# Kernel optimization log

Hardware: AMD Instinct MI355X
Metric: run time of the kernel (lower is better)

The kernel has to match this reference:

```python
import jax, jax.numpy as jnp
import numpy as np

B_, T_, DIN, H, DZ, DX = 64, 256, 128, 256, 8, 8


def setup_inputs() -> dict:
    key = jax.random.key(0)
    ks = jax.random.split(key, 13)
    p = lambda k, sh: jax.random.normal(k, sh, dtype=jnp.float32) * 0.05
    return {
        "y": jax.random.normal(ks[0], (B_, T_, DIN), dtype=jnp.float32),
        "W_ih": p(ks[1], (3 * H, DIN)), "W_hh": p(ks[2], (3 * H, H)),
        "b_ih": p(ks[3], (3 * H,)), "b_hh": p(ks[4], (3 * H,)),
        "W_mz": p(ks[5], (DZ, H)), "b_mz": p(ks[6], (DZ,)),
        "W_mx": p(ks[7], (DX, H)), "b_mx": p(ks[8], (DX,)),
        "W_pz": p(ks[9], (2 * DZ, H)), "b_pz": p(ks[10], (2 * DZ,)),
        "W_cx": p(ks[11], (DX * DX, H)), "b_cx": p(ks[12], (DX * DX,)),
    }


def _gru(y, W_ih, W_hh, b_ih, b_hh):
    # torch nn.GRU (single layer, unidirectional, batch_first)
    B, T, _ = y.shape
    Hh = W_hh.shape[1]
    x_proj = jnp.einsum('btd,gd->btg', y, W_ih) + b_ih  # [B,T,3H]

    def step(h, xp):
        hp = h @ W_hh.T + b_hh
        xr, xz, xn = jnp.split(xp, 3, axis=-1)
        hr, hz, hn = jnp.split(hp, 3, axis=-1)
        r = jax.nn.sigmoid(xr + hr)
        z = jax.nn.sigmoid(xz + hz)
        n = jnp.tanh(xn + r * hn)
        h_new = (1.0 - z) * n + z * h
        return h_new, h_new

    h0 = jnp.zeros((B, Hh), dtype=y.dtype)
    _, hs = jax.lax.scan(step, h0, jnp.swapaxes(x_proj, 0, 1))
    return jnp.swapaxes(hs, 0, 1)  # [B,T,H]


def _forward(y, W_ih, W_hh, b_ih, b_hh, W_mz, b_mz, W_mx, b_mx, W_pz, b_pz, W_cx, b_cx):
    enc = _gru(y, W_ih, W_hh, b_ih, b_hh)                       # [B,T,H]
    mean_z = enc @ W_mz.T + b_mz                                 # [B,T,DZ]
    mean_x = enc @ W_mx.T + b_mx                                 # [B,T,DX]
    bd_z = enc @ W_pz.T + b_pz                                   # [B,T,2*DZ]  (apply_softplus=False)

    # banded cov: per latent dim, upper-bidiagonal cholesky factor [B,T,T]
    diag = jnp.moveaxis(jax.nn.softplus(bd_z[..., :DZ]), -1, 0)  # [DZ,B,T]
    off = jnp.moveaxis(bd_z[:, :-1, DZ:], -1, 0)                 # [DZ,B,T-1]
    B, T = diag.shape[1], diag.shape[2]
    idx = jnp.arange(T)
    chol_z = (jnp.zeros((DZ, B, T, T), dtype=y.dtype)
              .at[:, :, idx, idx].set(diag)
              .at[:, :, idx[:-1], idx[1:]].set(off))             # [DZ,B,T,T]

    # anchor first two x-dims at t=0 (in-place mutation in torch)
    mean_x = mean_x.at[:, :, :2].add(-mean_x[:, 0:1, :2])
    mean_x_flat = mean_x.reshape(B * T, DX)

    cov_x = enc @ W_cx.T + b_cx                                  # [B,T,DX*DX]
    cov_x_flat = cov_x.reshape(B * T, DX, DX)
    return mean_z, chol_z, mean_x_flat, cov_x_flat


def reference(y, W_ih, W_hh, b_ih, b_hh, W_mz, b_mz, W_mx, b_mx, W_pz, b_pz, W_cx, b_cx):
    return _forward(y, W_ih, W_hh, b_ih, b_hh, W_mz, b_mz, W_mx, b_mx, W_pz, b_pz, W_cx, b_cx)
```

## Files before the change

kernel.cpp:

```cpp
#include <hip/hip_runtime.h>
#include <cstdint>
#include <cstddef>

#define B_   64
#define T_   256
#define DIN_ 128
#define H_   256
#define G3_  768

typedef _Float16 f16x8 __attribute__((ext_vector_type(8)));
typedef float    f32x4 __attribute__((ext_vector_type(4)));

#define MFMA(a, b, c) __builtin_amdgcn_mfma_f32_16x16x32_f16((a), (b), (c), 0, 0, 0)

__device__ __forceinline__ unsigned short f2h(float f) {
  _Float16 h = (_Float16)f;
  return __builtin_bit_cast(unsigned short, h);
}

__global__ __launch_bounds__(256) void prep_kernel(
    const float* __restrict__ W_ih, const float* __restrict__ W_hh,
    const float* __restrict__ W_mz, const float* __restrict__ W_mx,
    const float* __restrict__ W_pz, const float* __restrict__ W_cx,
    float* __restrict__ WT_ih, float* __restrict__ WheadT,
    unsigned* __restrict__ Wreg) {
  int i = blockIdx.x * 256 + threadIdx.x;
  if (i < 98304) {
    int k = i / 768, g = i % 768;
    WT_ih[i] = W_ih[g * 128 + k];
  } else if (i < 98304 + 24576) {
    int j = i - 98304;
    int c = j >> 8, k = j & 255;
    float v;
    if (c < 8)       v = W_mz[c * 256 + k];
    else if (c < 16) v = W_mx[(c - 8) * 256 + k];
    else if (c < 32) v = W_pz[(c - 16) * 256 + k];
    else             v = W_cx[(c - 32) * 256 + k];
    WheadT[j] = v;
  } else {
    int m = i - 122880;
    int c = m & 3, n = m >> 2;
    int tid = n & 511, j4 = n >> 9;
    int g   = j4 >> 4;
    int rem = j4 & 15;
    int uti = rem >> 3, kf = rem & 7;
    int wv = tid >> 6, l = tid & 63;
    int u = (2 * wv + uti) * 16 + (l & 15);
    int k = kf * 32 + ((l >> 4) << 3) + 2 * c;
    int row = g * 256 + u;
    unsigned short lo = f2h(W_hh[row * 256 + k]);
    unsigned short hi = f2h(W_hh[row * 256 + k + 1]);
    Wreg[m] = ((unsigned)hi << 16) | (unsigned)lo;
  }
}

__global__ __launch_bounds__(256) void xproj_kernel(
    const float* __restrict__ y, const float* __restrict__ WT_ih,
    const float* __restrict__ b_ih, const float* __restrict__ b_hh,
    float* __restrict__ xp) {
  __shared__ float ylds[64][132];
  int tid = threadIdx.x;
  int row0 = blockIdx.x * 64;
  const float4* y4 = (const float4*)(y + (size_t)row0 * DIN_);
#pragma unroll
  for (int i = 0; i < 8; ++i) {
    int idx = i * 256 + tid;
    float4 v = y4[idx];
    int r = idx >> 5, c4 = (idx & 31) * 4;
    ylds[r][c4 + 0] = v.x; ylds[r][c4 + 1] = v.y;
    ylds[r][c4 + 2] = v.z; ylds[r][c4 + 3] = v.w;
  }
  __syncthreads();
  int tx = tid & 15, ty = tid >> 4;
  for (int c = 0; c < 6; ++c) {
    int col0 = c * 128 + tx * 8;
    float acc[4][8];
#pragma unroll
    for (int a = 0; a < 4; ++a)
#pragma unroll
      for (int b = 0; b < 8; ++b) acc[a][b] = 0.f;
#pragma unroll 4
    for (int k = 0; k < 128; ++k) {
      float4 w0 = *(const float4*)&WT_ih[k * 768 + col0];
      float4 w1 = *(const float4*)&WT_ih[k * 768 + col0 + 4];
      float a0 = ylds[ty * 4 + 0][k], a1 = ylds[ty * 4 + 1][k];
      float a2 = ylds[ty * 4 + 2][k], a3 = ylds[ty * 4 + 3][k];
      acc[0][0] += a0 * w0.x; acc[0][1] += a0 * w0.y; acc[0][2] += a0 * w0.z; acc[0][3] += a0 * w0.w;
      acc[0][4] += a0 * w1.x; acc[0][5] += a0 * w1.y; acc[0][6] += a0 * w1.z; acc[0][7] += a0 * w1.w;
      acc[1][0] += a1 * w0.x; acc[1][1] += a1 * w0.y; acc[1][2] += a1 * w0.z; acc[1][3] += a1 * w0.w;
      acc[1][4] += a1 * w1.x; acc[1][5] += a1 * w1.y; acc[1][6] += a1 * w1.z; acc[1][7] += a1 * w1.w;
      acc[2][0] += a2 * w0.x; acc[2][1] += a2 * w0.y; acc[2][2] += a2 * w0.z; acc[2][3] += a2 * w0.w;
      acc[2][4] += a2 * w1.x; acc[2][5] += a2 * w1.y; acc[2][6] += a2 * w1.z; acc[2][7] += a2 * w1.w;
      acc[3][0] += a3 * w0.x; acc[3][1] += a3 * w0.y; acc[3][2] += a3 * w0.z; acc[3][3] += a3 * w0.w;
      acc[3][4] += a3 * w1.x; acc[3][5] += a3 * w1.y; acc[3][6] += a3 * w1.z; acc[3][7] += a3 * w1.w;
    }
    float4 b0 = *(const float4*)&b_ih[col0];
    float4 b1 = *(const float4*)&b_ih[col0 + 4];
    if (c < 4) {
      float4 h0 = *(const float4*)&b_hh[col0];
      float4 h1 = *(const float4*)&b_hh[col0 + 4];
      b0.x += h0.x; b0.y += h0.y; b0.z += h0.z; b0.w += h0.w;
      b1.x += h1.x; b1.y += h1.y; b1.z += h1.z; b1.w += h1.w;
    }
#pragma unroll
    for (int a = 0; a < 4; ++a) {
      int row = row0 + ty * 4 + a;
      float4 o0, o1;
      o0.x = acc[a][0] + b0.x; o0.y = acc[a][1] + b0.y; o0.z = acc[a][2] + b0.z; o0.w = acc[a][3] + b0.w;
      o1.x = acc[a][4] + b1.x; o1.y = acc[a][5] + b1.y; o1.z = acc[a][6] + b1.z; o1.w = acc[a][7] + b1.w;
      *(float4*)&xp[(size_t)row * G3_ + col0] = o0;
      *(float4*)&xp[(size_t)row * G3_ + col0 + 4] = o1;
    }
  }
}

#define GRU_STEP(PAR, xr0, xz0, xn0, xr1, xz1, xn1,                            \
                 nxr0, nxz0, nxn0, nxr1, nxz1, nxn1)                           \
  {                                                                            \
    asm volatile("" ::: "memory");            \
    const int tc = t + PAR;                                                    \
    const float* xq = xpb + (size_t)(tc + 1) * G3_;          \
    nxr0 = xq[u0]; nxz0 = xq[256 + u0]; nxn0 = xq[512 + u0];                   \
    nxr1 = xq[u1]; nxz1 = xq[256 + u1]; nxn1 = xq[512 + u1];                   \
    uint4 hq0 = h4[PAR * 32 + g16];                                            \
    f16x8 hf0 = __builtin_bit_cast(f16x8, hq0);                                \
    f32x4 aR0 = MFMA(hf0, wf[0],  z4);  f32x4 aR1 = MFMA(hf0, wf[8],  z4);     \
    f32x4 aZ0 = MFMA(hf0, wf[16], z4);  f32x4 aZ1 = MFMA(hf0, wf[24], z4);     \
    f32x4 aN0 = MFMA(hf0, wf[32], z4);  f32x4 aN1 = MFMA(hf0, wf[40], z4);     \
    _Pragma("unroll")                                                          \
    for (int kf = 1; kf < 8; ++kf) {                                           \
      uint4 hq = h4[PAR * 32 + kf * 4 + g16];                                  \
      f16x8 hk = __builtin_bit_cast(f16x8, hq);                                \
      aR0 = MFMA(hk, wf[kf],      aR0); aR1 = MFMA(hk, wf[8 + kf],  aR1);      \
      aZ0 = MFMA(hk, wf[16 + kf], aZ0); aZ1 = MFMA(hk, wf[24 + kf], aZ1);      \
      aN0 = MFMA(hk, wf[32 + kf], aN0); aN1 = MFMA(hk, wf[40 + kf], aN1);      \
    }                                                                          \
    float pr0 = aR0[0] + xr0, pz0 = aZ0[0] + xz0, pn0 = aN0[0] + bhn0;         \
    float pr1 = aR1[0] + xr1, pz1 = aZ1[0] + xz1, pn1 = aN1[0] + bhn1;         \
    float r0 = 1.f / (1.f + __expf(-pr0)), r1 = 1.f / (1.f + __expf(-pr1));    \
    float q0 = 1.f / (1.f + __expf(-pz0)), q1 = 1.f / (1.f + __expf(-pz1));    \
    float a0 = xn0 + r0 * pn0, a1 = xn1 + r1 * pn1;                            \
    a0 = fminf(15.f, fmaxf(-15.f, a0)); a1 = fminf(15.f, fmaxf(-15.f, a1));    \
    float e0 = __expf(2.f * a0), e1 = __expf(2.f * a1);                        \
    float n0 = (e0 - 1.f) / (e0 + 1.f), n1 = (e1 - 1.f) / (e1 + 1.f);          \
    float h0n = (1.f - q0) * n0 + q0 * hold0;                                  \
    float h1n = (1.f - q1) * n1 + q1 * hold1;                                  \
    hold0 = h0n; hold1 = h1n;                 \
    if ((l >> 4) == 0) {                        \
      encb[tc * 256 + u0] = h0n;  encb[tc * 256 + u1] = h1n;                   \
      h16[PAR ^ 1][u0] = f2h(h0n); h16[PAR ^ 1][u1] = f2h(h1n);                \
    }                                                                          \
    __syncthreads();                                                           \
  }

__global__ __launch_bounds__(512) __attribute__((amdgpu_waves_per_eu(2, 2)))
void gru_kernel(
    const float* __restrict__ xp, const unsigned* Wreg,
    const float* __restrict__ b_hh, float* enc) {
  int tid = threadIdx.x;
  int b = blockIdx.x;
  int w = tid >> 6;
  int l = tid & 63;
  int g16 = l >> 4;
  int u0 = w * 32 + (l & 15);
  int u1 = u0 + 16;
  __shared__ alignas(16) unsigned short h16[2][256];

  f16x8 wf[48];
  const uint4* W4 = (const uint4*)Wreg;
#pragma unroll
  for (int fi = 0; fi < 48; ++fi) {
    uint4 q = W4[fi * 512 + tid];
    wf[fi] = __builtin_bit_cast(f16x8, q);
  }
  if (tid < 32) {
    uint4 z = {0u, 0u, 0u, 0u};
    ((uint4*)h16)[tid] = z;
  }
  const float* xpb = xp + (size_t)b * (T_ * G3_);
  float* encb = enc + (size_t)b * (T_ * H_);
  float bhn0 = b_hh[512 + u0], bhn1 = b_hh[512 + u1];
  float hold0 = 0.f, hold1 = 0.f;
  const f32x4 z4 = {0.f, 0.f, 0.f, 0.f};
  float xrA0 = xpb[u0], xzA0 = xpb[256 + u0], xnA0 = xpb[512 + u0];
  float xrA1 = xpb[u1], xzA1 = xpb[256 + u1], xnA1 = xpb[512 + u1];
  __syncthreads();
  const uint4* h4 = (const uint4*)h16;
  float xrB0, xzB0, xnB0, xrB1, xzB1, xnB1;
  for (int t = 0; t < T_; t += 2) {
    GRU_STEP(0, xrA0, xzA0, xnA0, xrA1, xzA1, xnA1,
                xrB0, xzB0, xnB0, xrB1, xzB1, xnB1)
    GRU_STEP(1, xrB0, xzB0, xnB0, xrB1, xzB1, xnB1,
                xrA0, xzA0, xnA0, xrA1, xzA1, xnA1)
  }
}

__global__ __launch_bounds__(384) void heads_kernel(
    const float* __restrict__ enc, const float* __restrict__ WheadT,
    const float* __restrict__ b_mz, const float* __restrict__ b_mx,
    const float* __restrict__ b_pz, const float* __restrict__ b_cx,
    float* __restrict__ out_meanz, float* __restrict__ out_meanx,
    float* __restrict__ out_covx, float* __restrict__ stage,
    float4* __restrict__ chol4, float* __restrict__ anchor,
    const float* __restrict__ W_mx) {
  int tid = threadIdx.x;
  if (blockIdx.x >= 704) {
    __shared__ float red[4];
    int bid = blockIdx.x - 704;
    int b = bid >> 1, d = bid & 1;
    if (tid < 256) {
      float v = enc[(size_t)b * (T_ * H_) + tid] * W_mx[d * 256 + tid];
#pragma unroll
      for (int off = 32; off >= 1; off >>= 1) v += __shfl_down(v, off, 64);
      if ((tid & 63) == 0) red[tid >> 6] = v;
    }
    __syncthreads();
    if (tid == 0)
      anchor[b * 2 + d] = b_mx[d] + ((red[0] + red[1]) + (red[2] + red[3]));
    return;
  }
  if (blockIdx.x >= 512) {
    float4* cz = chol4 + 4194304;
    int idx = (blockIdx.x - 512) * 384 + tid;
    float4 z = {0.f, 0.f, 0.f, 0.f};
    for (; idx < 4194304; idx += 192 * 384) cz[idx] = z;
    return;
  }
  __shared__ float el[32 * 256];
  int row0 = blockIdx.x * 32;
  const float4* e4 = (const float4*)(enc + (size_t)row0 * 256);
  float4* el4 = (float4*)el;
#pragma unroll
  for (int i = 0; i < 6; ++i) {
    int idx = i * 384 + tid;
    if (idx < 2048) el4[idx] = e4[idx];
  }
  __syncthreads();
  int rg = tid / 96, c = tid - rg * 96;
  const float4* Wc = (const float4*)(WheadT + c * 256);
  float acc[8];
#pragma unroll
  for (int r = 0; r < 8; ++r) acc[r] = 0.f;
  for (int k4 = 0; k4 < 64; ++k4) {
    float4 w4 = Wc[k4];
#pragma unroll
    for (int r = 0; r < 8; ++r) {
      float4 ev = el4[(rg * 8 + r) * 64 + k4];
      acc[r] += w4.x * ev.x; acc[r] += w4.y * ev.y;
      acc[r] += w4.z * ev.z; acc[r] += w4.w * ev.w;
    }
  }
#pragma unroll
  for (int r = 0; r < 8; ++r) {
    int row = row0 + rg * 8 + r;
    float a_ = acc[r];
    if (c < 8) {
      out_meanz[(size_t)row * 8 + c] = a_ + b_mz[c];
    } else if (c < 16) {
      int d = c - 8;
      out_meanx[(size_t)row * 8 + d] = a_ + b_mx[d];
    } else if (c < 32) {
      int d = c - 16;
      float v = a_ + b_pz[d];
      if (d < 8)
        v = (v > 0.f) ? (v + log1pf(__expf(-v))) : log1pf(__expf(v));
      stage[(size_t)row * 16 + d] = v;
    } else {
      int d = c - 32;
      out_covx[(size_t)row * 64 + d] = a_ + b_cx[d];
    }
  }
}

__global__ __launch_bounds__(256) void chol_fin(
    const float* __restrict__ stage, float4* __restrict__ chol,
    const float* __restrict__ anchor, float* __restrict__ mean_x) {
  int i = blockIdx.x * 256 + threadIdx.x;
  int stride = gridDim.x * 256;
  for (; i < 4358144; i += stride) {
    if (i < 4194304) {
      int d = i >> 20;
      int bt = (i >> 6) & 16383;
      int t = bt & 255;
      int lane = i & 63;
      float vd = 0.f, vo = 0.f;
      if ((t >> 2) == lane)       vd = stage[bt * 16 + d];
      if (((t + 1) >> 2) == lane) vo = stage[bt * 16 + 8 + d];
      int te = t & 3, oe = (t + 1) & 3;
      float4 v;
      v.x = (te == 0 ? vd : 0.f) + (oe == 0 ? vo : 0.f);
      v.y = (te == 1 ? vd : 0.f) + (oe == 1 ? vo : 0.f);
      v.z = (te == 2 ? vd : 0.f) + (oe == 2 ? vo : 0.f);
      v.w = (te == 3 ? vd : 0.f) + (oe == 3 ? vo : 0.f);
      chol[i] = v;
    } else if (i < 4325376) {
      int j = i - 4194304;
      int bt = j >> 3, q = j & 7;
      int bb = bt >> 8, tt = bt & 255;
      int d = 4 + (q & 3);
      float* ch = (float*)chol;
      if (q < 4) {
        ch[(((size_t)d * 64 + bb) * 256 + tt) * 256 + tt] = stage[bt * 16 + d];
      } else if (tt < 255) {
        ch[(((size_t)d * 64 + bb) * 256 + tt) * 256 + tt + 1] = stage[bt * 16 + 8 + d];
      }
    } else {
      int j2 = i - 4325376;
      int row = j2 >> 1, d = j2 & 1;
      mean_x[(size_t)row * 8 + d] -= anchor[(row >> 8) * 2 + d];
    }
  }
}

extern "C" void kernel_launch(void* const* d_in, const int* in_sizes, int n_in,
                              void* d_out, int out_size, void* d_ws, size_t ws_size,
                              hipStream_t stream) {
  const float* y    = (const float*)d_in[0];
  const float* W_ih = (const float*)d_in[1];
  const float* W_hh = (const float*)d_in[2];
  const float* b_ih = (const float*)d_in[3];
  const float* b_hh = (const float*)d_in[4];
  const float* W_mz = (const float*)d_in[5];
  const float* b_mz = (const float*)d_in[6];
  const float* W_mx = (const float*)d_in[7];
  const float* b_mx = (const float*)d_in[8];
  const float* W_pz = (const float*)d_in[9];
  const float* b_pz = (const float*)d_in[10];
  const float* W_cx = (const float*)d_in[11];
  const float* b_cx = (const float*)d_in[12];

  float* out    = (float*)d_out;
  float* mean_z = out;
  float* chol   = out + 131072;
  float* mean_x = out + 33685504;
  float* cov_x  = out + 33816576;

  float* ws      = (float*)d_ws;
  float* WT_ih   = ws;
  float* WheadT  = ws + 98304;
  unsigned* Wreg = (unsigned*)(ws + 122880);
  float* anchor  = ws + 221184;
  float* stage   = ws + 221312;

  float* xp  = chol;
  float* enc = chol + 12582912;

  prep_kernel<<<864, 256, 0, stream>>>(W_ih, W_hh, W_mz, W_mx, W_pz, W_cx,
                                       WT_ih, WheadT, Wreg);
  xproj_kernel<<<256, 256, 0, stream>>>(y, WT_ih, b_ih, b_hh, xp);
  gru_kernel<<<64, 512, 0, stream>>>(xp, Wreg, b_hh, enc);
  heads_kernel<<<832, 384, 0, stream>>>(enc, WheadT, b_mz, b_mx, b_pz, b_cx,
                                        mean_z, mean_x, cov_x, stage,
                                        (float4*)chol, anchor, W_mx);
  chol_fin<<<4096, 256, 0, stream>>>(stage, (float4*)chol, anchor, mean_x);
}
```

Before: 597.7 us.

## Overlap chol zero-fill with GRU, split xproj columns, scatter band directly

Extra blocks added to the GRU launch zero the upper half of the chol output, so the fill runs on CUs the 64 recurrent blocks leave idle instead of inside the heads kernel. The heads kernel now writes the diagonal and off-diagonal values for latent dims 4-7 straight into chol, which removes that scatter pass from chol_fin. xproj is split across twice as many blocks, each computing half the gate columns, for more parallelism at the cost of loading y twice. The GRU gate arithmetic is reordered so z*h and 1-z are computed before the tanh. The zero-fill blocks may compete with the latency-bound GRU blocks for memory bandwidth.

```diff
diff --git a/kernel.cpp b/kernel.cpp
--- a/kernel.cpp
+++ b/kernel.cpp
@@ -60,7 +60,8 @@
     float* __restrict__ xp) {
   __shared__ float ylds[64][132];
   int tid = threadIdx.x;
-  int row0 = blockIdx.x * 64;
+  int row0 = (blockIdx.x >> 1) * 64;
+  int c0 = (blockIdx.x & 1) * 3;
   const float4* y4 = (const float4*)(y + (size_t)row0 * DIN_);
 #pragma unroll
   for (int i = 0; i < 8; ++i) {
@@ -72,7 +73,7 @@
   }
   __syncthreads();
   int tx = tid & 15, ty = tid >> 4;
-  for (int c = 0; c < 6; ++c) {
+  for (int c = c0; c < c0 + 3; ++c) {
     int col0 = c * 128 + tx * 8;
     float acc[4][8];
 #pragma unroll
@@ -135,16 +136,20 @@
       aZ0 = MFMA(hk, wf[16 + kf], aZ0); aZ1 = MFMA(hk, wf[24 + kf], aZ1);      \
       aN0 = MFMA(hk, wf[32 + kf], aN0); aN1 = MFMA(hk, wf[40 + kf], aN1);      \
     }                                                                          \
-    float pr0 = aR0[0] + xr0, pz0 = aZ0[0] + xz0, pn0 = aN0[0] + bhn0;         \
-    float pr1 = aR1[0] + xr1, pz1 = aZ1[0] + xz1, pn1 = aN1[0] + bhn1;         \
+             \
+    float pr0 = aR0[0] + xr0, pr1 = aR1[0] + xr1;                              \
+    float pz0 = aZ0[0] + xz0, pz1 = aZ1[0] + xz1;                              \
     float r0 = 1.f / (1.f + __expf(-pr0)), r1 = 1.f / (1.f + __expf(-pr1));    \
     float q0 = 1.f / (1.f + __expf(-pz0)), q1 = 1.f / (1.f + __expf(-pz1));    \
+    float zh0 = q0 * hold0, zh1 = q1 * hold1;                                  \
+    float om0 = 1.f - q0,   om1 = 1.f - q1;                                    \
+    float pn0 = aN0[0] + bhn0, pn1 = aN1[0] + bhn1;                            \
     float a0 = xn0 + r0 * pn0, a1 = xn1 + r1 * pn1;                            \
     a0 = fminf(15.f, fmaxf(-15.f, a0)); a1 = fminf(15.f, fmaxf(-15.f, a1));    \
     float e0 = __expf(2.f * a0), e1 = __expf(2.f * a1);                        \
     float n0 = (e0 - 1.f) / (e0 + 1.f), n1 = (e1 - 1.f) / (e1 + 1.f);          \
-    float h0n = (1.f - q0) * n0 + q0 * hold0;                                  \
-    float h1n = (1.f - q1) * n1 + q1 * hold1;                                  \
+    float h0n = om0 * n0 + zh0;                                                \
+    float h1n = om1 * n1 + zh1;                                                \
     hold0 = h0n; hold1 = h1n;                 \
     if ((l >> 4) == 0) {                        \
       encb[tc * 256 + u0] = h0n;  encb[tc * 256 + u1] = h1n;                   \
@@ -156,9 +161,15 @@
 __global__ __launch_bounds__(512) __attribute__((amdgpu_waves_per_eu(2, 2)))
 void gru_kernel(
     const float* __restrict__ xp, const unsigned* Wreg,
-    const float* __restrict__ b_hh, float* enc) {
+    const float* __restrict__ b_hh, float* enc, float4* __restrict__ cholU) {
   int tid = threadIdx.x;
   int b = blockIdx.x;
+  if (b >= 64) {
+    float4 zz = {0.f, 0.f, 0.f, 0.f};
+    int idx = (b - 64) * 512 + tid;
+    for (; idx < 4194304; idx += 98304) cholU[idx] = zz;
+    return;
+  }
   int w = tid >> 6;
   int l = tid & 63;
   int g16 = l >> 4;
@@ -201,12 +212,12 @@
     const float* __restrict__ b_pz, const float* __restrict__ b_cx,
     float* __restrict__ out_meanz, float* __restrict__ out_meanx,
     float* __restrict__ out_covx, float* __restrict__ stage,
-    float4* __restrict__ chol4, float* __restrict__ anchor,
+    float* __restrict__ chol, float* __restrict__ anchor,
     const float* __restrict__ W_mx) {
   int tid = threadIdx.x;
-  if (blockIdx.x >= 704) {
+  if (blockIdx.x >= 512) {
     __shared__ float red[4];
-    int bid = blockIdx.x - 704;
+    int bid = blockIdx.x - 512;
     int b = bid >> 1, d = bid & 1;
     if (tid < 256) {
       float v = enc[(size_t)b * (T_ * H_) + tid] * W_mx[d * 256 + tid];
@@ -217,13 +228,6 @@
     __syncthreads();
     if (tid == 0)
       anchor[b * 2 + d] = b_mx[d] + ((red[0] + red[1]) + (red[2] + red[3]));
-    return;
-  }
-  if (blockIdx.x >= 512) {
-    float4* cz = chol4 + 4194304;
-    int idx = (blockIdx.x - 512) * 384 + tid;
-    float4 z = {0.f, 0.f, 0.f, 0.f};
-    for (; idx < 4194304; idx += 192 * 384) cz[idx] = z;
     return;
   }
   __shared__ float el[32 * 256];
@@ -264,7 +268,18 @@
       float v = a_ + b_pz[d];
       if (d < 8)
         v = (v > 0.f) ? (v + log1pf(__expf(-v))) : log1pf(__expf(v));
-      stage[(size_t)row * 16 + d] = v;
+      int bb = row >> 8, tt = row & 255;
+      if (d < 4) {
+        stage[(size_t)row * 16 + d] = v;
+      } else if (d < 8) {
+        chol[(((size_t)d * 64 + bb) * 256 + tt) * 256 + tt] = v;
+      } else if (d < 12) {
+        stage[(size_t)row * 16 + d] = v;
+      } else {
+        int dd = d - 8;
+        if (tt < 255)
+          chol[(((size_t)dd * 64 + bb) * 256 + tt) * 256 + tt + 1] = v;
+      }
     } else {
       int d = c - 32;
       out_covx[(size_t)row * 64 + d] = a_ + b_cx[d];
@@ -277,7 +292,7 @@
     const float* __restrict__ anchor, float* __restrict__ mean_x) {
   int i = blockIdx.x * 256 + threadIdx.x;
   int stride = gridDim.x * 256;
-  for (; i < 4358144; i += stride) {
+  for (; i < 4227072; i += stride) {
     if (i < 4194304) {
       int d = i >> 20;
       int bt = (i >> 6) & 16383;
@@ -293,19 +308,8 @@
       v.z = (te == 2 ? vd : 0.f) + (oe == 2 ? vo : 0.f);
       v.w = (te == 3 ? vd : 0.f) + (oe == 3 ? vo : 0.f);
       chol[i] = v;
-    } else if (i < 4325376) {
-      int j = i - 4194304;
-      int bt = j >> 3, q = j & 7;
-      int bb = bt >> 8, tt = bt & 255;
-      int d = 4 + (q & 3);
-      float* ch = (float*)chol;
-      if (q < 4) {
-        ch[(((size_t)d * 64 + bb) * 256 + tt) * 256 + tt] = stage[bt * 16 + d];
-      } else if (tt < 255) {
-        ch[(((size_t)d * 64 + bb) * 256 + tt) * 256 + tt + 1] = stage[bt * 16 + 8 + d];
-      }
     } else {
-      int j2 = i - 4325376;
+      int j2 = i - 4194304;
       int row = j2 >> 1, d = j2 & 1;
       mean_x[(size_t)row * 8 + d] -= anchor[(row >> 8) * 2 + d];
     }
@@ -347,10 +351,11 @@
 
   prep_kernel<<<864, 256, 0, stream>>>(W_ih, W_hh, W_mz, W_mx, W_pz, W_cx,
                                        WT_ih, WheadT, Wreg);
-  xproj_kernel<<<256, 256, 0, stream>>>(y, WT_ih, b_ih, b_hh, xp);
-  gru_kernel<<<64, 512, 0, stream>>>(xp, Wreg, b_hh, enc);
-  heads_kernel<<<832, 384, 0, stream>>>(enc, WheadT, b_mz, b_mx, b_pz, b_cx,
+  xproj_kernel<<<512, 256, 0, stream>>>(y, WT_ih, b_ih, b_hh, xp);
+  gru_kernel<<<256, 512, 0, stream>>>(xp, Wreg, b_hh, enc,
+                                      ((float4*)chol) + 4194304);
+  heads_kernel<<<640, 384, 0, stream>>>(enc, WheadT, b_mz, b_mx, b_pz, b_cx,
                                         mean_z, mean_x, cov_x, stage,
-                                        (float4*)chol, anchor, W_mx);
+                                        chol, anchor, W_mx);
   chol_fin<<<4096, 256, 0, stream>>>(stage, (float4*)chol, anchor, mean_x);
 }
```

Measured after the change: 557.9 us. 6.7% less time.
